# Performance work log

Hardware: AMD Instinct MI355X
Metric: run time of the kernel (lower is better)

The kernel has to match this reference:

```python
import jax, jax.numpy as jnp
import numpy as np

N_NODES = 50000
N_EDGES = 1600000
IN_SIZE = 128
HIDDEN = 128
OUT_SIZE = 64
NUM_LAYERS = 3
BN_EPS = 1e-5
GIN_EPS_INIT = 1e-5


def setup_inputs() -> dict:
    key = jax.random.key(0)
    ks = jax.random.split(key, 16)
    node_feat = jax.random.normal(ks[0], (N_NODES, IN_SIZE), dtype=jnp.float32)
    src = jax.random.randint(ks[1], (N_EDGES,), 0, N_NODES)
    dst = jax.random.randint(ks[2], (N_EDGES,), 0, N_NODES)
    # per-layer MLP params (in_size == hidden, so shapes are uniform across layers)
    s1 = 1.0 / np.sqrt(IN_SIZE)
    s2 = 1.0 / np.sqrt(HIDDEN)
    W1 = jax.random.uniform(ks[3], (NUM_LAYERS, IN_SIZE, HIDDEN), jnp.float32, -s1, s1)
    b1 = jax.random.uniform(ks[4], (NUM_LAYERS, HIDDEN), jnp.float32, -s1, s1)
    gamma = jnp.ones((NUM_LAYERS, HIDDEN), jnp.float32)
    beta = jnp.zeros((NUM_LAYERS, HIDDEN), jnp.float32)
    W2 = jax.random.uniform(ks[5], (NUM_LAYERS, HIDDEN, HIDDEN), jnp.float32, -s2, s2)
    b2 = jax.random.uniform(ks[6], (NUM_LAYERS, HIDDEN), jnp.float32, -s2, s2)
    eps = jnp.full((NUM_LAYERS,), GIN_EPS_INIT, jnp.float32)  # learnable GIN eps
    Wout = jax.random.uniform(ks[7], (HIDDEN, OUT_SIZE), jnp.float32, -s2, s2)
    bout = jax.random.uniform(ks[8], (OUT_SIZE,), jnp.float32, -s2, s2)
    return {"node_feat": node_feat, "src": src, "dst": dst,
            "W1": W1, "b1": b1, "gamma": gamma, "beta": beta,
            "W2": W2, "b2": b2, "eps": eps, "Wout": Wout, "bout": bout}


def reference(node_feat, src, dst, W1, b1, gamma, beta, W2, b2, eps, Wout, bout):
    n = node_feat.shape[0]
    h = node_feat
    for i in range(NUM_LAYERS):
        # sum-aggregate source features onto destination nodes
        agg = jax.ops.segment_sum(h[src], dst, num_segments=n)  # [N, d]
        x = (1.0 + eps[i]) * h + agg
        x = x @ W1[i] + b1[i]
        # BatchNorm1d (training mode: batch statistics, biased variance)
        mu = jnp.mean(x, axis=0)
        var = jnp.var(x, axis=0)
        x = (x - mu) * jax.lax.rsqrt(var + BN_EPS) * gamma[i] + beta[i]
        x = jax.nn.relu(x)
        h = jax.nn.relu(x @ W2[i] + b2[i])
    return h @ Wout + bout
```

## Files before the change

kernel.cpp:

```cpp
#include <hip/hip_runtime.h>

#define NN 50000
#define NE 1600000
#define HID 128
#define NB 196
#define BCAP 12288

typedef _Float16 half8 __attribute__((ext_vector_type(8)));
typedef float floatx4 __attribute__((ext_vector_type(4)));


__global__ __launch_bounds__(256) void kb_count(const int* __restrict__ dst,
                                                int* __restrict__ gcnt, int E) {
  __shared__ int cnt[NB];
  int tid = threadIdx.x;
  for (int i = tid; i < NB; i += 256) cnt[i] = 0;
  __syncthreads();
  int base = blockIdx.x * 4096;
  for (int i = 0; i < 16; ++i) {
    int e = base + i * 256 + tid;
    if (e < E) atomicAdd(&cnt[dst[e] >> 8], 1);
  }
  __syncthreads();
  for (int i = tid; i < NB; i += 256)
    if (cnt[i]) atomicAdd(&gcnt[i], cnt[i]);
}

__global__ __launch_bounds__(256) void kb_basescan(const int* __restrict__ gcnt,
                                                   int* __restrict__ bbase,
                                                   int* __restrict__ bcur) {
  __shared__ int s[256];
  int tid = threadIdx.x;
  int v = (tid < NB) ? gcnt[tid] : 0;
  s[tid] = v;
  __syncthreads();
  for (int d = 1; d < 256; d <<= 1) {
    int t = (tid >= d) ? s[tid - d] : 0;
    __syncthreads();
    s[tid] += t;
    __syncthreads();
  }
  int incl = s[tid];
  if (tid < NB) {
    bbase[tid] = incl - v;
    bcur[tid] = incl - v;
  }
  if (tid == NB - 1) bbase[NB] = incl;
}

__global__ __launch_bounds__(256) void kb_partition(const int* __restrict__ src,
                                                    const int* __restrict__ dst,
                                                    int* __restrict__ bcur,
                                                    int2* __restrict__ ebuf, int E) {
  __shared__ int cnt[NB];
  __shared__ int sbase[NB];
  int tid = threadIdx.x;
  for (int i = tid; i < NB; i += 256) cnt[i] = 0;
  __syncthreads();
  int base = blockIdx.x * 4096;
  int myd[16], mys[16];
#pragma unroll
  for (int i = 0; i < 16; ++i) {
    int e = base + i * 256 + tid;
    if (e < E) {
      myd[i] = dst[e];
      mys[i] = src[e];
      atomicAdd(&cnt[myd[i] >> 8], 1);
    } else {
      myd[i] = -1;
    }
  }
  __syncthreads();
  for (int i = tid; i < NB; i += 256)
    sbase[i] = cnt[i] ? atomicAdd(&bcur[i], cnt[i]) : 0;
  __syncthreads();
  for (int i = tid; i < NB; i += 256) cnt[i] = 0;
  __syncthreads();
#pragma unroll
  for (int i = 0; i < 16; ++i) {
    if (myd[i] >= 0) {
      int b = myd[i] >> 8;
      int r = atomicAdd(&cnt[b], 1);
      ebuf[sbase[b] + r] = make_int2(mys[i], myd[i]);
    }
  }
}

__global__ __launch_bounds__(256) void kb_csr(const int2* __restrict__ ebuf,
                                              const int* __restrict__ bbase,
                                              int* __restrict__ rs,
                                              int* __restrict__ eidx, int M) {
  __shared__ int cnt[256];
  __shared__ int off[256];
  __shared__ int sbuf[BCAP];
  int tid = threadIdx.x;
  int b = blockIdx.x;
  int lo = bbase[b], hi = bbase[b + 1];
  int n = hi - lo;
  cnt[tid] = 0;
  __syncthreads();
  for (int i = tid; i < n; i += 256) atomicAdd(&cnt[ebuf[lo + i].y & 255], 1);
  __syncthreads();
  int v = cnt[tid];
  off[tid] = v;
  __syncthreads();
  for (int d = 1; d < 256; d <<= 1) {
    int t = (tid >= d) ? off[tid - d] : 0;
    __syncthreads();
    off[tid] += t;
    __syncthreads();
  }
  int excl = off[tid] - v;
  int gnode = b * 256 + tid;
  if (gnode < M) rs[gnode] = lo + excl;
  if (b == NB - 1 && tid == 0) rs[M] = bbase[NB];
  __syncthreads();
  cnt[tid] = excl;
  __syncthreads();
  if (n <= BCAP) {
    for (int i = tid; i < n; i += 256) {
      int2 ed = ebuf[lo + i];
      int r = atomicAdd(&cnt[ed.y & 255], 1);
      sbuf[r] = ed.x;
    }
    __syncthreads();
    for (int i = tid; i < n; i += 256) eidx[lo + i] = sbuf[i];
  } else {
    for (int i = tid; i < n; i += 256) {
      int2 ed = ebuf[lo + i];
      int r = atomicAdd(&cnt[ed.y & 255], 1);
      eidx[lo + r] = ed.x;
    }
  }
}


__global__ __launch_bounds__(256) void k_cvt(const float* __restrict__ x,
                                             _Float16* __restrict__ y, int n8) {
  int t = blockIdx.x * 256 + threadIdx.x;
  if (t >= n8) return;
  const float4* x4 = (const float4*)x;
  float4 u = x4[t * 2], v = x4[t * 2 + 1];
  half8 o;
  o[0] = (_Float16)u.x; o[1] = (_Float16)u.y; o[2] = (_Float16)u.z; o[3] = (_Float16)u.w;
  o[4] = (_Float16)v.x; o[5] = (_Float16)v.y; o[6] = (_Float16)v.z; o[7] = (_Float16)v.w;
  ((half8*)y)[t] = o;
}


__global__ __launch_bounds__(256) void k_pack(const float* __restrict__ W1,
                                              const float* __restrict__ W2,
                                              const float* __restrict__ Wout,
                                              _Float16* __restrict__ wp) {
  int y = blockIdx.y;
  const float* W;
  _Float16* dst;
  int NCT;
  if (y < 3) { W = W1 + (size_t)y * 16384; dst = wp + y * 16384; NCT = 8; }
  else if (y < 6) { W = W2 + (size_t)(y - 3) * 16384; dst = wp + 49152 + (y - 3) * 16384; NCT = 8; }
  else { W = Wout; dst = wp + 98304; NCT = 4; }
  int t = blockIdx.x * 256 + threadIdx.x;
  if (t >= 4 * NCT * 64) return;
  int lane = t & 63;
  int ct = (t >> 6) % NCT;
  int kb = t / (64 * NCT);
  int n = ct * 16 + (lane & 15);
  int k0 = kb * 32 + (lane >> 4) * 8;
  int N = NCT * 16;
#pragma unroll
  for (int j = 0; j < 8; ++j) dst[t * 8 + j] = (_Float16)W[(k0 + j) * N + n];
}


__global__ __launch_bounds__(1024, 8) void k_aggemm1(
    const int* __restrict__ rs, const int* __restrict__ eidx,
    const float* __restrict__ eps, int layer, const _Float16* __restrict__ h,
    const _Float16* __restrict__ wp1, const float* __restrict__ b1L,
    float* __restrict__ csum, float* __restrict__ csq,
    _Float16* __restrict__ x) {
  __shared__ _Float16 As[64 * 136];
  __shared__ float sredS[512];
  __shared__ float sredQ[512];
  const int tid = threadIdx.x;
  const int wid = tid >> 6;
  const int lane = tid & 63;
  const int slot = lane >> 4;
  const int c8 = lane & 15;
  const int c8t = tid & 15;
  const int rowBase = blockIdx.x * 64;
  const float ep = 1.0f + eps[layer];
  const half8* h8 = (const half8*)h;

  for (int i = 0; i < 4; ++i) {
    const int node = rowBase + wid * 4 + i;
    float a0[8] = {0, 0, 0, 0, 0, 0, 0, 0};
    float a1[8] = {0, 0, 0, 0, 0, 0, 0, 0};
    float a2[8] = {0, 0, 0, 0, 0, 0, 0, 0};
    float a3[8] = {0, 0, 0, 0, 0, 0, 0, 0};
    int e0 = 0, e1 = 0;
    if (node < NN) {
      e0 = rs[node];
      e1 = rs[node + 1];
    }
    int e = e0 + slot;
    for (; e + 12 < e1; e += 16) {
      int s0 = eidx[e];
      int s1 = eidx[e + 4];
      int s2 = eidx[e + 8];
      int s3 = eidx[e + 12];
      half8 v0 = h8[s0 * 16 + c8];
      half8 v1 = h8[s1 * 16 + c8];
      half8 v2 = h8[s2 * 16 + c8];
      half8 v3 = h8[s3 * 16 + c8];
#pragma unroll
      for (int j = 0; j < 8; ++j) {
        a0[j] += (float)v0[j];
        a1[j] += (float)v1[j];
        a2[j] += (float)v2[j];
        a3[j] += (float)v3[j];
      }
    }
    for (; e < e1; e += 4) {
      half8 v = h8[eidx[e] * 16 + c8];
#pragma unroll
      for (int j = 0; j < 8; ++j) a0[j] += (float)v[j];
    }
#pragma unroll
    for (int j = 0; j < 8; ++j) {
      a0[j] += a1[j] + a2[j] + a3[j];
      a0[j] += __shfl_xor(a0[j], 16);
      a0[j] += __shfl_xor(a0[j], 32);
    }
    if (slot == 0) {
      half8 o = {0, 0, 0, 0, 0, 0, 0, 0};
      if (node < NN) {
        half8 hv = h8[node * 16 + c8];
#pragma unroll
        for (int j = 0; j < 8; ++j) o[j] = (_Float16)fmaf(ep, (float)hv[j], a0[j]);
      }
      *(half8*)(As + (wid * 4 + i) * 136 + c8 * 8) = o;
    }
  }
  __syncthreads();

  const int rg = wid & 3;
  const int cg = wid >> 2;
  floatx4 acc[2];
  acc[0] = (floatx4){0.f, 0.f, 0.f, 0.f};
  acc[1] = (floatx4){0.f, 0.f, 0.f, 0.f};
  const half8* wp8 = (const half8*)wp1;
#pragma unroll
  for (int kb = 0; kb < 4; ++kb) {
    half8 a = *(const half8*)(As + (rg * 16 + c8) * 136 + kb * 32 + slot * 8);
#pragma unroll
    for (int t = 0; t < 2; ++t) {
      int ct = cg * 2 + t;
      acc[t] = __builtin_amdgcn_mfma_f32_16x16x32_f16(a, wp8[(kb * 8 + ct) * 64 + lane],
                                                      acc[t], 0, 0, 0);
    }
  }
  __syncthreads();

#pragma unroll
  for (int t = 0; t < 2; ++t) {
    int ct = cg * 2 + t;
    float bv = b1L[ct * 16 + c8];
    float ps = 0.f, pq = 0.f;
#pragma unroll
    for (int reg = 0; reg < 4; ++reg) {
      int row = rg * 16 + slot * 4 + reg;
      float xv = acc[t][reg] + bv;
      As[row * 136 + ct * 16 + c8] = (_Float16)xv;
      if (rowBase + row < NN) {
        ps += xv;
        pq += xv * xv;
      }
    }
    ps += __shfl_xor(ps, 16);
    ps += __shfl_xor(ps, 32);
    pq += __shfl_xor(pq, 16);
    pq += __shfl_xor(pq, 32);
    if (lane < 16) {
      sredS[wid * 32 + t * 16 + lane] = ps;
      sredQ[wid * 32 + t * 16 + lane] = pq;
    }
  }
  __syncthreads();

  {
    int row = tid >> 4;
    int gr = rowBase + row;
    if (gr < NN) {
      half8 v = *(half8*)(As + row * 136 + c8t * 8);
      *(half8*)(x + (size_t)gr * 128 + c8t * 8) = v;
    }
  }
  if (tid < 128) {
    int c = tid;
    int wbase = (c >> 5) * 4;
    int loc = c & 31;
    float s = sredS[wbase * 32 + loc] + sredS[(wbase + 1) * 32 + loc] +
              sredS[(wbase + 2) * 32 + loc] + sredS[(wbase + 3) * 32 + loc];
    atomicAdd(&csum[c], s);
  } else if (tid < 256) {
    int c = tid - 128;
    int wbase = (c >> 5) * 4;
    int loc = c & 31;
    float q = sredQ[wbase * 32 + loc] + sredQ[(wbase + 1) * 32 + loc] +
              sredQ[(wbase + 2) * 32 + loc] + sredQ[(wbase + 3) * 32 + loc];
    atomicAdd(&csq[c], q);
  }
}


template <int FINAL>
__global__ __launch_bounds__(1024, 8) void k_bn_gemm2(
    const _Float16* __restrict__ x, const _Float16* __restrict__ wp2,
    const float* __restrict__ b2L, const float* __restrict__ gammaL,
    const float* __restrict__ betaL, const float* __restrict__ csum,
    const float* __restrict__ csq, _Float16* __restrict__ hout,
    const _Float16* __restrict__ wpo, const float* __restrict__ boutp,
    float* __restrict__ out) {
  __shared__ _Float16 As[64 * 136];
  const int tid = threadIdx.x;
  const int wid = tid >> 6;
  const int lane = tid & 63;
  const int slot = lane >> 4;
  const int c8 = lane & 15;
  const int c8t = tid & 15;
  const int rowBase = blockIdx.x * 64;

  float sc[8], sh[8];
  {
    const float invM = 1.0f / (float)NN;
#pragma unroll
    for (int j = 0; j < 8; ++j) {
      int k = c8t * 8 + j;
      float mu = csum[k] * invM;
      float var = csq[k] * invM - mu * mu;
      float g = gammaL[k] * rsqrtf(var + 1e-5f);
      sc[j] = g;
      sh[j] = fmaf(-mu, g, betaL[k]);
    }
  }
  {
    int row = tid >> 4;
    int gr = rowBase + row;
    half8 v = {0, 0, 0, 0, 0, 0, 0, 0};
    if (gr < NN) {
      v = *(const half8*)(x + (size_t)gr * 128 + c8t * 8);
#pragma unroll
      for (int j = 0; j < 8; ++j)
        v[j] = (_Float16)fmaxf(fmaf((float)v[j], sc[j], sh[j]), 0.f);
    }
    *(half8*)(As + row * 136 + c8t * 8) = v;
  }
  __syncthreads();

  const int rg = wid & 3;
  const int cg = wid >> 2;
  floatx4 acc[2];
  acc[0] = (floatx4){0.f, 0.f, 0.f, 0.f};
  acc[1] = (floatx4){0.f, 0.f, 0.f, 0.f};
  const half8* wp8 = (const half8*)wp2;
#pragma unroll
  for (int kb = 0; kb < 4; ++kb) {
    half8 a = *(const half8*)(As + (rg * 16 + c8) * 136 + kb * 32 + slot * 8);
#pragma unroll
    for (int t = 0; t < 2; ++t) {
      int ct = cg * 2 + t;
      acc[t] = __builtin_amdgcn_mfma_f32_16x16x32_f16(a, wp8[(kb * 8 + ct) * 64 + lane],
                                                      acc[t], 0, 0, 0);
    }
  }
  __syncthreads();
#pragma unroll
  for (int t = 0; t < 2; ++t) {
    int ct = cg * 2 + t;
    float bv = b2L[ct * 16 + c8];
#pragma unroll
    for (int reg = 0; reg < 4; ++reg) {
      int row = rg * 16 + slot * 4 + reg;
      As[row * 136 + ct * 16 + c8] = (_Float16)fmaxf(acc[t][reg] + bv, 0.f);
    }
  }
  __syncthreads();

  if (FINAL == 0) {
    int row = tid >> 4;
    int gr = rowBase + row;
    if (gr < NN) {
      half8 v = *(half8*)(As + row * 136 + c8t * 8);
      *(half8*)(hout + (size_t)gr * 128 + c8t * 8) = v;
    }
  } else {
    if (cg < 2) {
      floatx4 acc3[2];
      acc3[0] = (floatx4){0.f, 0.f, 0.f, 0.f};
      acc3[1] = (floatx4){0.f, 0.f, 0.f, 0.f};
      const half8* wo8 = (const half8*)wpo;
#pragma unroll
      for (int kb = 0; kb < 4; ++kb) {
        half8 a = *(const half8*)(As + (rg * 16 + c8) * 136 + kb * 32 + slot * 8);
#pragma unroll
        for (int t = 0; t < 2; ++t) {
          int ct = cg * 2 + t;
          acc3[t] = __builtin_amdgcn_mfma_f32_16x16x32_f16(
              a, wo8[(kb * 4 + ct) * 64 + lane], acc3[t], 0, 0, 0);
        }
      }
#pragma unroll
      for (int t = 0; t < 2; ++t) {
        int ct = cg * 2 + t;
        float bv = boutp[ct * 16 + c8];
#pragma unroll
        for (int reg = 0; reg < 4; ++reg) {
          int gr = rowBase + rg * 16 + slot * 4 + reg;
          if (gr < NN) out[(size_t)gr * 64 + ct * 16 + c8] = acc3[t][reg] + bv;
        }
      }
    }
  }
}


extern "C" void kernel_launch(void* const* d_in, const int* in_sizes, int n_in,
                              void* d_out, int out_size, void* d_ws, size_t ws_size,
                              hipStream_t stream) {
  const float* node_feat = (const float*)d_in[0];
  const int* src = (const int*)d_in[1];
  const int* dst = (const int*)d_in[2];
  const float* W1 = (const float*)d_in[3];
  const float* b1 = (const float*)d_in[4];
  const float* gamma = (const float*)d_in[5];
  const float* beta = (const float*)d_in[6];
  const float* W2 = (const float*)d_in[7];
  const float* b2 = (const float*)d_in[8];
  const float* eps = (const float*)d_in[9];
  const float* Wout = (const float*)d_in[10];
  const float* bout = (const float*)d_in[11];
  float* out = (float*)d_out;

  int* rs = (int*)d_ws;
  int* gcnt = rs + 50176;
  int* bbase = gcnt + 256;
  int* bcur = bbase + 256;
  float* stats = (float*)(bcur + 256);
  int* eidx = (int*)(stats + 768);
  _Float16* hb = (_Float16*)(eidx + NE);
  _Float16* xb = hb + (size_t)NN * HID;
  _Float16* wp = xb + (size_t)NN * HID;
  int2* ebuf = (int2*)(wp + 106496);

  hipMemsetAsync(gcnt, 0, (256 * 3 + 768) * sizeof(int), stream);

  k_cvt<<<(NN * HID / 8 + 255) / 256, 256, 0, stream>>>(node_feat, hb, NN * HID / 8);
  k_pack<<<dim3(8, 7), 256, 0, stream>>>(W1, W2, Wout, wp);

  const int partGrid = (NE + 4095) / 4096;
  kb_count<<<partGrid, 256, 0, stream>>>(dst, gcnt, NE);
  kb_basescan<<<1, 256, 0, stream>>>(gcnt, bbase, bcur);
  kb_partition<<<partGrid, 256, 0, stream>>>(src, dst, bcur, ebuf, NE);
  kb_csr<<<NB, 256, 0, stream>>>(ebuf, bbase, rs, eidx, NN);

  const int rowTiles = (NN + 63) / 64;

  for (int L = 0; L < 3; ++L) {
    float* csum = stats + L * 256;
    float* csq = csum + 128;
    k_aggemm1<<<rowTiles, 1024, 0, stream>>>(
        rs, eidx, eps, L, hb, wp + (size_t)L * 16384, b1 + (size_t)L * HID,
        csum, csq, xb);
    if (L < 2) {
      k_bn_gemm2<0><<<rowTiles, 1024, 0, stream>>>(
          xb, wp + 49152 + (size_t)L * 16384, b2 + (size_t)L * HID,
          gamma + (size_t)L * HID, beta + (size_t)L * HID, csum, csq, hb,
          nullptr, nullptr, nullptr);
    } else {
      k_bn_gemm2<1><<<rowTiles, 1024, 0, stream>>>(
          xb, wp + 49152 + (size_t)L * 16384, b2 + (size_t)L * HID,
          gamma + (size_t)L * HID, beta + (size_t)L * HID, csum, csq, nullptr,
          wp + 98304, bout, out);
    }
  }
}
```

Measured before the change: 443.9 us.

## Pack edge buffer into single int and split gather into column passes

Edge partition entries now pack the source index and the low 8 destination bits into one int, which halves ebuf traffic in partition and CSR build. The aggregation in k_aggemm1 now walks each node's edges four times, each pass covering a 64-byte column slice (4 lanes per row, 16 edges in flight per wavefront), instead of one pass over full 256-byte rows with 4 edges in flight. The aim is more memory-level parallelism and cache locality on the gathered rows. The cost is re-reading eidx four times, more shuffle reductions, and source indices limited to 24 bits.

```diff
diff --git a/kernel.cpp b/kernel.cpp
--- a/kernel.cpp
+++ b/kernel.cpp
@@ -51,7 +51,7 @@
 __global__ __launch_bounds__(256) void kb_partition(const int* __restrict__ src,
                                                     const int* __restrict__ dst,
                                                     int* __restrict__ bcur,
-                                                    int2* __restrict__ ebuf, int E) {
+                                                    int* __restrict__ ebuf, int E) {
   __shared__ int cnt[NB];
   __shared__ int sbase[NB];
   int tid = threadIdx.x;
@@ -81,12 +81,12 @@
     if (myd[i] >= 0) {
       int b = myd[i] >> 8;
       int r = atomicAdd(&cnt[b], 1);
-      ebuf[sbase[b] + r] = make_int2(mys[i], myd[i]);
-    }
-  }
-}
-
-__global__ __launch_bounds__(256) void kb_csr(const int2* __restrict__ ebuf,
+      ebuf[sbase[b] + r] = (mys[i] << 8) | (myd[i] & 255);
+    }
+  }
+}
+
+__global__ __launch_bounds__(256) void kb_csr(const int* __restrict__ ebuf,
                                               const int* __restrict__ bbase,
                                               int* __restrict__ rs,
                                               int* __restrict__ eidx, int M) {
@@ -99,7 +99,7 @@
   int n = hi - lo;
   cnt[tid] = 0;
   __syncthreads();
-  for (int i = tid; i < n; i += 256) atomicAdd(&cnt[ebuf[lo + i].y & 255], 1);
+  for (int i = tid; i < n; i += 256) atomicAdd(&cnt[ebuf[lo + i] & 255], 1);
   __syncthreads();
   int v = cnt[tid];
   off[tid] = v;
@@ -119,17 +119,17 @@
   __syncthreads();
   if (n <= BCAP) {
     for (int i = tid; i < n; i += 256) {
-      int2 ed = ebuf[lo + i];
-      int r = atomicAdd(&cnt[ed.y & 255], 1);
-      sbuf[r] = ed.x;
+      int ed = ebuf[lo + i];
+      int r = atomicAdd(&cnt[ed & 255], 1);
+      sbuf[r] = ed >> 8;
     }
     __syncthreads();
     for (int i = tid; i < n; i += 256) eidx[lo + i] = sbuf[i];
   } else {
     for (int i = tid; i < n; i += 256) {
-      int2 ed = ebuf[lo + i];
-      int r = atomicAdd(&cnt[ed.y & 255], 1);
-      eidx[lo + r] = ed.x;
+      int ed = ebuf[lo + i];
+      int r = atomicAdd(&cnt[ed & 255], 1);
+      eidx[lo + r] = ed >> 8;
     }
   }
 }
@@ -187,58 +187,58 @@
   const int slot = lane >> 4;
   const int c8 = lane & 15;
   const int c8t = tid & 15;
+  const int eslot = lane >> 2;
+  const int col4 = lane & 3;
   const int rowBase = blockIdx.x * 64;
   const float ep = 1.0f + eps[layer];
   const half8* h8 = (const half8*)h;
 
-  for (int i = 0; i < 4; ++i) {
-    const int node = rowBase + wid * 4 + i;
-    float a0[8] = {0, 0, 0, 0, 0, 0, 0, 0};
-    float a1[8] = {0, 0, 0, 0, 0, 0, 0, 0};
-    float a2[8] = {0, 0, 0, 0, 0, 0, 0, 0};
-    float a3[8] = {0, 0, 0, 0, 0, 0, 0, 0};
-    int e0 = 0, e1 = 0;
-    if (node < NN) {
-      e0 = rs[node];
-      e1 = rs[node + 1];
-    }
-    int e = e0 + slot;
-    for (; e + 12 < e1; e += 16) {
-      int s0 = eidx[e];
-      int s1 = eidx[e + 4];
-      int s2 = eidx[e + 8];
-      int s3 = eidx[e + 12];
-      half8 v0 = h8[s0 * 16 + c8];
-      half8 v1 = h8[s1 * 16 + c8];
-      half8 v2 = h8[s2 * 16 + c8];
-      half8 v3 = h8[s3 * 16 + c8];
+#pragma unroll
+  for (int p = 0; p < 4; ++p) {
+    const int pc = p * 4;
+    for (int i = 0; i < 4; ++i) {
+      const int node = rowBase + wid * 4 + i;
+      float a0[8] = {0, 0, 0, 0, 0, 0, 0, 0};
+      float a1[8] = {0, 0, 0, 0, 0, 0, 0, 0};
+      int e0 = 0, e1 = 0;
+      if (node < NN) {
+        e0 = rs[node];
+        e1 = rs[node + 1];
+      }
+      int e = e0 + eslot;
+      for (; e + 16 < e1; e += 32) {
+        int s0 = eidx[e];
+        int s1 = eidx[e + 16];
+        half8 v0 = h8[s0 * 16 + pc + col4];
+        half8 v1 = h8[s1 * 16 + pc + col4];
+#pragma unroll
+        for (int j = 0; j < 8; ++j) {
+          a0[j] += (float)v0[j];
+          a1[j] += (float)v1[j];
+        }
+      }
+      if (e < e1) {
+        half8 v = h8[eidx[e] * 16 + pc + col4];
+#pragma unroll
+        for (int j = 0; j < 8; ++j) a0[j] += (float)v[j];
+      }
 #pragma unroll
       for (int j = 0; j < 8; ++j) {
-        a0[j] += (float)v0[j];
-        a1[j] += (float)v1[j];
-        a2[j] += (float)v2[j];
-        a3[j] += (float)v3[j];
-      }
-    }
-    for (; e < e1; e += 4) {
-      half8 v = h8[eidx[e] * 16 + c8];
-#pragma unroll
-      for (int j = 0; j < 8; ++j) a0[j] += (float)v[j];
-    }
-#pragma unroll
-    for (int j = 0; j < 8; ++j) {
-      a0[j] += a1[j] + a2[j] + a3[j];
-      a0[j] += __shfl_xor(a0[j], 16);
-      a0[j] += __shfl_xor(a0[j], 32);
-    }
-    if (slot == 0) {
-      half8 o = {0, 0, 0, 0, 0, 0, 0, 0};
-      if (node < NN) {
-        half8 hv = h8[node * 16 + c8];
-#pragma unroll
-        for (int j = 0; j < 8; ++j) o[j] = (_Float16)fmaf(ep, (float)hv[j], a0[j]);
-      }
-      *(half8*)(As + (wid * 4 + i) * 136 + c8 * 8) = o;
+        a0[j] += a1[j];
+        a0[j] += __shfl_xor(a0[j], 4);
+        a0[j] += __shfl_xor(a0[j], 8);
+        a0[j] += __shfl_xor(a0[j], 16);
+        a0[j] += __shfl_xor(a0[j], 32);
+      }
+      if (eslot == 0) {
+        half8 o = {0, 0, 0, 0, 0, 0, 0, 0};
+        if (node < NN) {
+          half8 hv = h8[node * 16 + pc + col4];
+#pragma unroll
+          for (int j = 0; j < 8; ++j) o[j] = (_Float16)fmaf(ep, (float)hv[j], a0[j]);
+        }
+        *(half8*)(As + (wid * 4 + i) * 136 + (pc + col4) * 8) = o;
+      }
     }
   }
   __syncthreads();
@@ -450,7 +450,7 @@
   _Float16* hb = (_Float16*)(eidx + NE);
   _Float16* xb = hb + (size_t)NN * HID;
   _Float16* wp = xb + (size_t)NN * HID;
-  int2* ebuf = (int2*)(wp + 106496);
+  int* ebuf = (int*)(wp + 106496);
 
   hipMemsetAsync(gcnt, 0, (256 * 3 + 768) * sizeof(int), stream);
 
```

Result: slower. 561.4 us (+26.5%).
